# Kernel tuning notes

Measured on AMD Instinct MI355X. Metric: run time of the kernel, lower is better.

The kernel has to match this reference:

```python
import jax, jax.numpy as jnp
import numpy as np

UNITS = 1024
N_CLASSES = 41
SUBSAMPLE = 4
KERNEL = 3
FEAT = 256


def setup_inputs() -> dict:
    key = jax.random.key(0)
    ks = jax.random.split(key, 12)
    B, T, F, U, C = 32, 1000, FEAT, UNITS, N_CLASSES
    s = lambda k, shape, sc: jax.random.normal(k, shape, dtype=jnp.float32) * sc
    return {
        "x": jax.random.normal(ks[0], (B, T, F), dtype=jnp.float32),
        # depthwise conv kernel: (width, 1, channels) for WIO with groups=C
        "conv_w": s(ks[1], (KERNEL, 1, F), 0.1),
        "h0_init": s(ks[2], (1, U), 0.05),
        "w0_x": s(ks[3], (F, 3 * U), 1.0 / np.sqrt(F)),
        "w0_h": s(ks[4], (U, 3 * U), 1.0 / np.sqrt(U)),
        "b0": jnp.zeros((2, 3 * U), dtype=jnp.float32),
        "w1_x": s(ks[5], (U, 3 * U), 1.0 / np.sqrt(U)),
        "w1_h": s(ks[6], (U, 3 * U), 1.0 / np.sqrt(U)),
        "b1": jnp.zeros((2, 3 * U), dtype=jnp.float32),
        "dense_w": s(ks[7], (U, C), 1.0 / np.sqrt(U)),
        "dense_b": jnp.zeros((C,), dtype=jnp.float32),
    }


def _depthwise_conv1d(x, w):
    # x: [B, T, C], w: [K, 1, C]; SAME padding, groups = C, relu, no bias
    C = x.shape[-1]
    y = jax.lax.conv_general_dilated(
        x, w, window_strides=(1,), padding="SAME",
        dimension_numbers=("NWC", "WIO", "NWC"), feature_group_count=C)
    return jax.nn.relu(y)


def _gru_layer(x, h0, Wx, Wh, b):
    # Keras GRU v2 (reset_after=True), gate order z, r, h.
    # x: [B, T, F]; h0: [B, U]; Wx: [F, 3U]; Wh: [U, 3U]; b: [2, 3U]
    xproj = jnp.einsum("btf,fg->btg", x, Wx) + b[0]  # [B, T, 3U]
    br = b[1]

    def step(h, xp):
        rec = h @ Wh + br  # [B, 3U]
        xz, xr, xh = jnp.split(xp, 3, axis=-1)
        rz, rr, rh = jnp.split(rec, 3, axis=-1)
        z = jax.nn.sigmoid(xz + rz)
        r = jax.nn.sigmoid(xr + rr)
        hh = jnp.tanh(xh + r * rh)
        hn = z * h + (1.0 - z) * hh
        return hn, hn

    _, ys = jax.lax.scan(step, h0, jnp.swapaxes(xproj, 0, 1))  # [T, B, U]
    return jnp.swapaxes(ys, 0, 1)


def reference(x, conv_w, h0_init, w0_x, w0_h, b0, w1_x, w1_h, b1, dense_w, dense_b):
    B = x.shape[0]
    U = w0_h.shape[0]
    h = _depthwise_conv1d(x, conv_w)
    # layer 0: learned initial state tiled over batch
    h = _gru_layer(h, jnp.tile(h0_init, (B, 1)), w0_x, w0_h, b0)
    # subsample after layer nLayers-2 == 0
    h = h[:, ::SUBSAMPLE, :]
    # layer 1: zero initial state (Keras default when initial_state is None)
    h = _gru_layer(h, jnp.zeros((B, U), dtype=x.dtype), w1_x, w1_h, b1)
    return h @ dense_w + dense_b  # [B, T//4, nClasses]
```

## Files before the change

kernel.cpp:

```cpp
#include <hip/hip_runtime.h>

typedef unsigned int u32;
typedef unsigned long long u64;
typedef unsigned short u16;
typedef __attribute__((ext_vector_type(8))) short short8;
typedef __attribute__((ext_vector_type(4))) float f32x4;
typedef __attribute__((ext_vector_type(4))) unsigned int u32x4;

#define MFMA(a,b,c) __builtin_amdgcn_mfma_f32_16x16x32_bf16((a),(b),(c),0,0,0)
#define ALOAD32(p)    __hip_atomic_load((p), __ATOMIC_RELAXED, __HIP_MEMORY_SCOPE_AGENT)
#define ASTORE32(p,v) __hip_atomic_store((p),(v), __ATOMIC_RELAXED, __HIP_MEMORY_SCOPE_AGENT)

__device__ __forceinline__ float bf2f(u32 b){ union{u32 u; float f;} v; v.u = b<<16; return v.f; }
__device__ __forceinline__ u16 f2bf(float f){ union{float f; u32 u;} v; v.f = f; u32 u = v.u;
  return (u16)((u + 0x7fffu + ((u>>16)&1u)) >> 16); }
__device__ __forceinline__ u32 pack_f(float v){
  u16 hi = f2bf(v); u16 lo = f2bf(v - bf2f(hi)); return (u32)hi | ((u32)lo<<16); }

__device__ __forceinline__ void unpack8(uint4 a, uint4 b, short8& hi, short8& lo){
  u32 w[8] = {a.x,a.y,a.z,a.w,b.x,b.y,b.z,b.w};
#pragma unroll
  for (int j=0;j<8;++j){ hi[j] = (short)(w[j] & 0xffffu); lo[j] = (short)(w[j] >> 16); }
}
__device__ __forceinline__ void unpackh4(u32x4 a, short8& hi){
#pragma unroll
  for (int i=0;i<4;++i){ hi[2*i] = (short)(a[i] & 0xffffu); hi[2*i+1] = (short)(a[i] >> 16); }
}

constexpr size_t OFF_Y    = 0;
constexpr size_t OFF_SUB  = 32768000;
constexpr size_t OFF_W0IH = 65536000;
constexpr size_t OFF_W0IL = 73400320;
constexpr size_t OFF_W1IH = 81264640;
constexpr size_t OFF_W1IL = 93847552;
constexpr size_t OFF_HB0  = 106430464;
constexpr size_t OFF_HB1  = 106692608;
constexpr size_t OFF_FL0  = 106954752;
constexpr size_t OFF_FL1  = 106955776;
constexpr size_t WS_NEED  = 106956800;

__global__ void build_w0img(const float* __restrict__ w0x, const float* __restrict__ w0h,
                            u16* __restrict__ imgH, u16* __restrict__ imgL){
  for (size_t i = (size_t)blockIdx.x*blockDim.x + threadIdx.x; i < 64ull*61440ull;
       i += (size_t)gridDim.x*blockDim.x){
    int wid = (int)(i / 61440), e = (int)(i % 61440);
    int e2, colbase; const float* src;
    if      (e < 4096) { e2 = e;         colbase = 0;    src = w0x; }
    else if (e < 8192) { e2 = e - 4096;  colbase = 1024; src = w0x; }
    else if (e < 24576){ e2 = e - 8192;  colbase = 0;    src = w0h; }
    else if (e < 40960){ e2 = e - 24576; colbase = 1024; src = w0h; }
    else if (e < 45056){ e2 = e - 40960; colbase = 2048; src = w0x; }
    else               { e2 = e - 45056; colbase = 2048; src = w0h; }
    int blk = e2 >> 9, r = e2 & 511;
    int kseg = r >> 7, c = (r >> 3) & 15, j = r & 7;
    int k = blk*32 + kseg*8 + j;
    int col = colbase + wid*16 + c;
    float v = src[(size_t)k*3072 + col];
    u16 hi = f2bf(v);
    imgH[i] = hi; imgL[i] = f2bf(v - bf2f(hi));
  }
}

__global__ void build_w1img(const float* __restrict__ w1x, const float* __restrict__ w1h,
                            u16* __restrict__ imgH, u16* __restrict__ imgL){
  for (size_t i = (size_t)blockIdx.x*blockDim.x + threadIdx.x; i < 128ull*49152ull;
       i += (size_t)gridDim.x*blockDim.x){
    int wid = (int)(i / 49152), e = (int)(i % 49152);
    int rg = e >> 14, e2 = e & 16383;
    int blk = e2 >> 9, rr = e2 & 511;
    int kseg = rr >> 7, c = (rr >> 3) & 15, j = rr & 7;
    int k = blk*32 + kseg*8 + j;
    const float* src; int col;
    if (rg == 0){ src = w1x; col = (c<8) ? (wid*8+c) : (1024 + wid*8 + c-8); }
    else if (rg == 1){ src = w1h; col = (c<8) ? (wid*8+c) : (1024 + wid*8 + c-8); }
    else { col = 2048 + wid*8 + ((c<8) ? c : c-8); src = (c<8) ? w1x : w1h; }
    float v = src[(size_t)k*3072 + col];
    u16 hi = f2bf(v);
    imgH[i] = hi; imgL[i] = f2bf(v - bf2f(hi));
  }
}

__global__ void init_state(const float* __restrict__ h0, u32* hb0, u32* hb1,
                           int* f0, int* f1){
  int i = blockIdx.x*blockDim.x + threadIdx.x;
  if (i < 256){ f0[i]=0; f1[i]=0; }
  if (i < 16384){
    int p = i & 511;
    u32 v = (u32)f2bf(h0[2*p]) | ((u32)f2bf(h0[2*p+1]) << 16);
    hb0[i] = v;
    hb1[i] = 0u;
  }
}

__global__ void conv_pack(const float* __restrict__ x, const float* __restrict__ cw,
                          u32* __restrict__ yp){
  for (size_t i = (size_t)blockIdx.x*blockDim.x + threadIdx.x; i < 8192000ull;
       i += (size_t)gridDim.x*blockDim.x){
    int f = (int)(i & 255); int b = (int)((i>>8)&31); int t = (int)(i>>13);
    const float* xb = x + ((size_t)b*1000 + t)*256 + f;
    float acc = xb[0]*cw[256+f];
    if (t > 0)   acc += xb[-256]*cw[f];
    if (t < 999) acc += xb[256]*cw[512+f];
    acc = fmaxf(acc, 0.0f);
    yp[i] = pack_f(acc);
  }
}

__global__ __launch_bounds__(512, 1)
void gru16_persist(const u32* __restrict__ xin,
                   const u16* __restrict__ imgH, const u16* __restrict__ imgL,
                   const float* __restrict__ bias,
                   u32* hbuf, int* flags, u32* out_pack)
{
  __shared__ u16 WIMG[61440];
  __shared__ float exch[8*8*66];
  __shared__ float harr[128];
  __shared__ int hready[32];

  const int tid  = threadIdx.x;
  const int wg   = blockIdx.x;
  const int g    = wg >> 6;
  const int wid  = wg & 63;
  const int lane = tid & 63;
  const int wave = tid >> 6;
  const int kq   = wave;
  const int lo16 = lane & 15, hi16 = lane >> 4;
  const int lane_off = hi16*128 + lo16*8;
  const int hsel = (kq >= 4) ? 16 : 0;
  const int srow = lo16 & 7;

  {
    const u64* sH = (const u64*)(imgH + (size_t)wid*61440);
    u64* dH = (u64*)WIMG;
    for (int i = tid; i < 15360; i += 512) dH[i] = sH[i];
    if (tid < 32) hready[tid] = 0;
    if (tid < 128){
      u16 hv = ((const u16*)hbuf)[g*8192 + (tid>>4)*1024 + wid*16 + (tid&15)];
      harr[tid] = bf2f((u32)hv);
    }
  }
  __syncthreads();

  const u16* gLo  = imgL + (size_t)wid*61440;
  const u16* zx_h = &WIMG[kq*512 + lane_off];          const u16* zx_l = gLo + kq*512 + lane_off;
  const u16* rx_h = &WIMG[4096 + kq*512 + lane_off];   const u16* rx_l = gLo + 4096 + kq*512 + lane_off;
  const u16* zh_h = &WIMG[8192 + kq*2048 + lane_off];  const u16* zh_l = gLo + 8192 + kq*2048 + lane_off;
  const u16* rh_h = &WIMG[24576 + kq*2048 + lane_off]; const u16* rh_l = gLo + 24576 + kq*2048 + lane_off;
  const u16* xh_h = &WIMG[40960 + kq*512 + lane_off];  const u16* xh_l = gLo + 40960 + kq*512 + lane_off;
  const u16* hh_h = &WIMG[45056 + kq*2048 + lane_off]; const u16* hh_l = gLo + 45056 + kq*2048 + lane_off;

  const int gs = tid >> 4, gu = tid & 15, eu = wid*16 + gu;
  const float zb  = bias[eu]        + bias[3072 + eu];
  const float rbv = bias[1024 + eu] + bias[4096 + eu];
  const float hxb = bias[2048 + eu];
  const float hrb = bias[5120 + eu];

  for (int t = 0; t < 1000; ++t) {
    const int cur = t & 1, nxt = cur ^ 1;
    f32x4 aZ  = (f32x4){0.f,0.f,0.f,0.f};
    f32x4 aR  = (f32x4){0.f,0.f,0.f,0.f};
    f32x4 aHX = (f32x4){0.f,0.f,0.f,0.f};
    f32x4 aHR = (f32x4){0.f,0.f,0.f,0.f};
    {
      const u32* xr = xin + ((size_t)t*32 + g*8 + srow)*256 + kq*32 + hi16*8;
      uint4 a0 = *(const uint4*)xr;
      uint4 a1 = *(const uint4*)(xr + 4);
      short8 ahi, alo; unpack8(a0, a1, ahi, alo);
      short8 bzh = *(const short8*)zx_h, bzl = *(const short8*)zx_l;
      short8 brh = *(const short8*)rx_h, brl = *(const short8*)rx_l;
      short8 bxh = *(const short8*)xh_h, bxl = *(const short8*)xh_l;
      aZ  = MFMA(ahi,bzh,aZ);  aZ  = MFMA(alo,bzh,aZ);  aZ  = MFMA(ahi,bzl,aZ);
      aR  = MFMA(ahi,brh,aR);  aR  = MFMA(alo,brh,aR);  aR  = MFMA(ahi,brl,aR);
      aHX = MFMA(ahi,bxh,aHX); aHX = MFMA(alo,bxh,aHX); aHX = MFMA(ahi,bxl,aHX);
    }
    if (t > 0) {
      if (wave == 0) {
        int f0;
        do { f0 = ALOAD32(flags + g*64 + (lane & 31)); } while (__all(f0 >= t) == 0);
        asm volatile("" ::: "memory");
        if (lane == 0) ((volatile int*)hready)[0] = t;
      } else if (wave == 1) {
        int f1;
        do { f1 = ALOAD32(flags + g*64 + 32 + (lane & 31)); } while (__all(f1 >= t) == 0);
        asm volatile("" ::: "memory");
        if (lane == 0) ((volatile int*)hready)[16] = t;
      }
      while (((volatile int*)hready)[hsel] < t) { }
      asm volatile("" ::: "memory");
    }
    {
      const u32* hrow = hbuf + cur*16384 + g*4096 + srow*512 + kq*64 + hi16*4;
      u32x4 qa, qb, qc, qd;
      asm volatile(
        "global_load_dwordx4 %0, %4, off sc0 sc1\n\t"
        "global_load_dwordx4 %1, %4, off offset:64 sc0 sc1\n\t"
        "global_load_dwordx4 %2, %4, off offset:128 sc0 sc1\n\t"
        "global_load_dwordx4 %3, %4, off offset:192 sc0 sc1\n\t"
        "s_waitcnt vmcnt(0)"
        : "=&v"(qa), "=&v"(qb), "=&v"(qc), "=&v"(qd)
        : "v"(hrow)
        : "memory");
      short8 ah0, ah1, ah2, ah3;
      unpackh4(qa, ah0); unpackh4(qb, ah1); unpackh4(qc, ah2); unpackh4(qd, ah3);
#pragma unroll
      for (int kt = 0; kt < 4; ++kt){
        short8 ah = (kt==0)?ah0:(kt==1)?ah1:(kt==2)?ah2:ah3;
        short8 bzh = *(const short8*)(zh_h + kt*512), bzl = *(const short8*)(zh_l + kt*512);
        short8 brh = *(const short8*)(rh_h + kt*512), brl = *(const short8*)(rh_l + kt*512);
        short8 bhh = *(const short8*)(hh_h + kt*512), bhl = *(const short8*)(hh_l + kt*512);
        aZ  = MFMA(ah,bzh,aZ);  aZ  = MFMA(ah,bzl,aZ);
        aR  = MFMA(ah,brh,aR);  aR  = MFMA(ah,brl,aR);
        aHR = MFMA(ah,bhh,aHR); aHR = MFMA(ah,bhl,aHR);
      }
    }
    {
      if (hi16 < 2) {
#pragma unroll
        for (int r4 = 0; r4 < 4; ++r4){
          float* e = &exch[(kq*8 + hi16*4 + r4)*66];
          e[lo16]      = aZ[r4];
          e[16 + lo16] = aR[r4];
          e[32 + lo16] = aHX[r4];
          e[48 + lo16] = aHR[r4];
        }
      }
    }
    __syncthreads();
    u32 pk_out = 0;
    if (tid < 128) {
      float zp=0.f, rp=0.f, xh=0.f, rh=0.f;
#pragma unroll
      for (int k8 = 0; k8 < 8; ++k8){
        const float* e = &exch[(k8*8 + gs)*66];
        zp += e[gu]; rp += e[16+gu]; xh += e[32+gu]; rh += e[48+gu];
      }
      float z = 1.f/(1.f + __expf(-(zp + zb)));
      float r = 1.f/(1.f + __expf(-(rp + rbv)));
      float pre = xh + hxb + r*(rh + hrb);
      float ex = __expf(-2.f*fabsf(pre));
      float th = (1.f - ex)/(1.f + ex);
      float hh = copysignf(th, pre);
      float hn = z*harr[tid] + (1.f - z)*hh;
      harr[tid] = hn;
      pk_out = pack_f(hn);
      int pk16 = (int)(pk_out & 0xffffu);
      int prt  = __shfl_xor(pk16, 1);
      if ((tid & 1) == 0) {
        u32 pair = (u32)pk16 | ((u32)prt << 16);
        ASTORE32(hbuf + nxt*16384 + g*4096 + gs*512 + wid*8 + (gu>>1), pair);
      }
    }
    asm volatile("s_waitcnt vmcnt(0)" ::: "memory");
    __syncthreads();
    if (tid == 0)
      ASTORE32(flags + g*64 + wid, t+1);
    if (tid < 128) {
      if ((t & 3) == 0)
        out_pack[((size_t)(t>>2)*32 + g*8 + gs)*1024 + eu] = pk_out;
    }
  }
}

__global__ __launch_bounds__(512, 1)
void gru8L1_persist(const u32* __restrict__ xin,
                    const u16* __restrict__ imgH, const u16* __restrict__ imgL,
                    const float* __restrict__ bias,
                    u32* hbuf, int* flags, u32* out_pack)
{
  __shared__ u16 WIMG[49152];
  __shared__ float exch[8*16*33];
  __shared__ float harr[128];
  __shared__ int hready[32];

  const int tid  = threadIdx.x;
  const int wg   = blockIdx.x;
  const int g    = wg >> 7;
  const int wid  = wg & 127;
  const int lane = tid & 63;
  const int wave = tid >> 6;
  const int kq   = wave;
  const int lo16 = lane & 15, hi16 = lane >> 4;
  const int lane_off = hi16*128 + lo16*8;
  const int hsel = (kq >= 4) ? 16 : 0;

  {
    const u64* sH = (const u64*)(imgH + (size_t)wid*49152);
    u64* dH = (u64*)WIMG;
    for (int i = tid; i < 12288; i += 512) dH[i] = sH[i];
    if (tid < 32) hready[tid] = 0;
    if (tid < 128){
      u16 hv = ((const u16*)hbuf)[g*16384 + (tid>>3)*1024 + wid*8 + (tid&7)];
      harr[tid] = bf2f((u32)hv);
    }
  }
  __syncthreads();

  const u16* gLo   = imgL + (size_t)wid*49152;
  const u16* zrx_h = &WIMG[kq*2048 + lane_off];          const u16* zrx_l = gLo + kq*2048 + lane_off;
  const u16* zrh_h = &WIMG[16384 + kq*2048 + lane_off];  const u16* zrh_l = gLo + 16384 + kq*2048 + lane_off;
  const u16* xhh_h = &WIMG[32768 + kq*2048 + lane_off];  const u16* xhh_l = gLo + 32768 + kq*2048 + lane_off;

  const int gs = tid >> 3, gu = tid & 7, eu = wid*8 + gu;
  const float zb  = bias[eu]        + bias[3072 + eu];
  const float rbv = bias[1024 + eu] + bias[4096 + eu];
  const float hxb = bias[2048 + eu];
  const float hrb = bias[5120 + eu];

  for (int t = 0; t < 250; ++t) {
    const int cur = t & 1, nxt = cur ^ 1;
    f32x4 aZR = (f32x4){0.f,0.f,0.f,0.f};
    f32x4 aXH = (f32x4){0.f,0.f,0.f,0.f};
    f32x4 aHR = (f32x4){0.f,0.f,0.f,0.f};
    {
      const u32* xrow = xin + ((size_t)t*32 + g*16 + lo16)*1024 + kq*128 + hi16*8;
#pragma unroll
      for (int kt = 0; kt < 4; ++kt) {
        uint4 a0 = *(const uint4*)(xrow + kt*32);
        uint4 a1 = *(const uint4*)(xrow + kt*32 + 4);
        short8 ahi, alo; unpack8(a0, a1, ahi, alo);
        short8 bzh = *(const short8*)(zrx_h + kt*512), bzl = *(const short8*)(zrx_l + kt*512);
        short8 bxh = *(const short8*)(xhh_h + kt*512), bxl = *(const short8*)(xhh_l + kt*512);
        aZR = MFMA(ahi,bzh,aZR); aZR = MFMA(alo,bzh,aZR); aZR = MFMA(ahi,bzl,aZR);
        aXH = MFMA(ahi,bxh,aXH); aXH = MFMA(alo,bxh,aXH); aXH = MFMA(ahi,bxl,aXH);
      }
    }
    if (t > 0) {
      if (wave == 0) {
        int f0;
        do { f0 = ALOAD32(flags + g*128 + lane); } while (__all(f0 >= t) == 0);
        asm volatile("" ::: "memory");
        if (lane == 0) ((volatile int*)hready)[0] = t;
      } else if (wave == 1) {
        int f1;
        do { f1 = ALOAD32(flags + g*128 + 64 + lane); } while (__all(f1 >= t) == 0);
        asm volatile("" ::: "memory");
        if (lane == 0) ((volatile int*)hready)[16] = t;
      }
      while (((volatile int*)hready)[hsel] < t) { }
      asm volatile("" ::: "memory");
    }
    {
      const u32* hrow = hbuf + cur*16384 + g*8192 + lo16*512 + kq*64 + hi16*4;
      u32x4 qa, qb, qc, qd;
      asm volatile(
        "global_load_dwordx4 %0, %4, off sc0 sc1\n\t"
        "global_load_dwordx4 %1, %4, off offset:64 sc0 sc1\n\t"
        "global_load_dwordx4 %2, %4, off offset:128 sc0 sc1\n\t"
        "global_load_dwordx4 %3, %4, off offset:192 sc0 sc1\n\t"
        "s_waitcnt vmcnt(0)"
        : "=&v"(qa), "=&v"(qb), "=&v"(qc), "=&v"(qd)
        : "v"(hrow)
        : "memory");
      short8 ah0, ah1, ah2, ah3;
      unpackh4(qa, ah0); unpackh4(qb, ah1); unpackh4(qc, ah2); unpackh4(qd, ah3);
#pragma unroll
      for (int kt = 0; kt < 4; ++kt){
        short8 ah = (kt==0)?ah0:(kt==1)?ah1:(kt==2)?ah2:ah3;
        short8 bzh = *(const short8*)(zrh_h + kt*512), bzl = *(const short8*)(zrh_l + kt*512);
        short8 bhh = *(const short8*)(xhh_h + kt*512), bhl = *(const short8*)(xhh_l + kt*512);
        aZR = MFMA(ah,bzh,aZR); aZR = MFMA(ah,bzl,aZR);
        aHR = MFMA(ah,bhh,aHR); aHR = MFMA(ah,bhl,aHR);
      }
    }
    {
#pragma unroll
      for (int r4 = 0; r4 < 4; ++r4){
        float* e = &exch[(kq*16 + hi16*4 + r4)*33];
        e[lo16]      = aZR[r4];
        e[16 + lo16] = (lo16 < 8) ? aXH[r4] : aHR[r4];
      }
    }
    __syncthreads();
    u32 pk_out = 0;
    if (tid < 128) {
      float zp=0.f, rp=0.f, xh=0.f, rh=0.f;
#pragma unroll
      for (int k8 = 0; k8 < 8; ++k8){
        const float* e = &exch[(k8*16 + gs)*33];
        zp += e[gu]; rp += e[8+gu]; xh += e[16+gu]; rh += e[24+gu];
      }
      float z = 1.f/(1.f + __expf(-(zp + zb)));
      float r = 1.f/(1.f + __expf(-(rp + rbv)));
      float pre = xh + hxb + r*(rh + hrb);
      float ex = __expf(-2.f*fabsf(pre));
      float th = (1.f - ex)/(1.f + ex);
      float hh = copysignf(th, pre);
      float hn = z*harr[tid] + (1.f - z)*hh;
      harr[tid] = hn;
      pk_out = pack_f(hn);
      int pk16 = (int)(pk_out & 0xffffu);
      int prt  = __shfl_xor(pk16, 1);
      if ((tid & 1) == 0) {
        u32 pair = (u32)pk16 | ((u32)prt << 16);
        ASTORE32(hbuf + nxt*16384 + g*8192 + gs*512 + wid*4 + (gu>>1), pair);
      }
    }
    asm volatile("s_waitcnt vmcnt(0)" ::: "memory");
    __syncthreads();
    if (tid == 0)
      ASTORE32(flags + g*128 + wid, t+1);
    if (tid < 128) {
      out_pack[((size_t)t*32 + g*16 + gs)*1024 + eu] = pk_out;
    }
  }
}

__global__ __launch_bounds__(256, 1)
void dense_k(const u32* __restrict__ h2, const float* __restrict__ W,
             const float* __restrict__ bias, float* __restrict__ out){
  __shared__ float rows[32*1025];
  const int ts = blockIdx.x;
  const u32* src = h2 + (size_t)ts*32768;
  for (int i = threadIdx.x; i < 32768; i += 256){
    u32 p = src[i];
    rows[(i>>10)*1025 + (i&1023)] = bf2f(p & 0xffffu) + bf2f(p >> 16);
  }
  __syncthreads();
  const int b = threadIdx.x >> 3, cg = threadIdx.x & 7;
  float acc[6] = {0.f,0.f,0.f,0.f,0.f,0.f};
  for (int k = 0; k < 1024; ++k){
    float hv = rows[b*1025 + k];
    const float* wr = W + k*41;
#pragma unroll
    for (int j = 0; j < 6; ++j){ int c = cg + 8*j; if (c < 41) acc[j] += hv*wr[c]; }
  }
#pragma unroll
  for (int j = 0; j < 6; ++j){
    int c = cg + 8*j;
    if (c < 41) out[((size_t)b*250 + ts)*41 + c] = acc[j] + bias[c];
  }
}

extern "C" void kernel_launch(void* const* d_in, const int* in_sizes, int n_in,
                              void* d_out, int out_size, void* d_ws, size_t ws_size,
                              hipStream_t stream) {
  const float* x      = (const float*)d_in[0];
  const float* conv_w = (const float*)d_in[1];
  const float* h0i    = (const float*)d_in[2];
  const float* w0x    = (const float*)d_in[3];
  const float* w0h    = (const float*)d_in[4];
  const float* b0     = (const float*)d_in[5];
  const float* w1x    = (const float*)d_in[6];
  const float* w1h    = (const float*)d_in[7];
  const float* b1     = (const float*)d_in[8];
  const float* dw     = (const float*)d_in[9];
  const float* db     = (const float*)d_in[10];
  float* outp = (float*)d_out;

  if (ws_size < WS_NEED) return;

  char* ws = (char*)d_ws;
  u32* y_pack   = (u32*)(ws + OFF_Y);
  u32* out2     = (u32*)(ws + OFF_Y);
  u32* sub_pack = (u32*)(ws + OFF_SUB);
  u16* w0iH = (u16*)(ws + OFF_W0IH); u16* w0iL = (u16*)(ws + OFF_W0IL);
  u16* w1iH = (u16*)(ws + OFF_W1IH); u16* w1iL = (u16*)(ws + OFF_W1IL);
  u32* hb0 = (u32*)(ws + OFF_HB0);
  u32* hb1 = (u32*)(ws + OFF_HB1);
  int* fl0 = (int*)(ws + OFF_FL0);
  int* fl1 = (int*)(ws + OFF_FL1);

  init_state<<<64, 512, 0, stream>>>(h0i, hb0, hb1, fl0, fl1);
  build_w0img<<<2048, 256, 0, stream>>>(w0x, w0h, w0iH, w0iL);
  build_w1img<<<2048, 256, 0, stream>>>(w1x, w1h, w1iH, w1iL);
  conv_pack<<<4096, 256, 0, stream>>>(x, conv_w, y_pack);

  gru16_persist<<<256, 512, 0, stream>>>(y_pack, w0iH, w0iL, b0, hb0, fl0, sub_pack);
  gru8L1_persist<<<256, 512, 0, stream>>>(sub_pack, w1iH, w1iL, b1, hb1, fl1, out2);

  dense_k<<<250, 256, 0, stream>>>(out2, dw, db, outp);
}
```

Measured before the change: 5.423 ms.

## Replace second per-step block barrier with LDS flag handshakes in persistent GRU

Removes the trailing __syncthreads after the gate computation in both persistent GRU kernels. In its place it uses LDS flags: the two gate waves signal when they have consumed the exchange buffer, and wave 1 signals when its hidden-state stores have drained. The publish to the global flag is then done by thread 0 after a spin on that signal, and the other waves only wait on the exchange-buffer flag before writing the next step. This shortens the serial per-timestep critical path, at the cost of more subtle spin-based ordering that relies on volatile LDS accesses.

```diff
diff --git a/kernel.cpp b/kernel.cpp
--- a/kernel.cpp
+++ b/kernel.cpp
@@ -106,6 +106,8 @@
   }
 }
 
+#define HREADY_INIT(idx) ((idx)==8 || (idx)==24 || (idx)==25 ? -1 : 0)
+
 __global__ __launch_bounds__(512, 1)
 void gru16_persist(const u32* __restrict__ xin,
                    const u16* __restrict__ imgH, const u16* __restrict__ imgL,
@@ -128,12 +130,13 @@
   const int lane_off = hi16*128 + lo16*8;
   const int hsel = (kq >= 4) ? 16 : 0;
   const int srow = lo16 & 7;
+  volatile int* vh = (volatile int*)hready;
 
   {
     const u64* sH = (const u64*)(imgH + (size_t)wid*61440);
     u64* dH = (u64*)WIMG;
     for (int i = tid; i < 15360; i += 512) dH[i] = sH[i];
-    if (tid < 32) hready[tid] = 0;
+    if (tid < 32) hready[tid] = HREADY_INIT(tid);
     if (tid < 128){
       u16 hv = ((const u16*)hbuf)[g*8192 + (tid>>4)*1024 + wid*16 + (tid&15)];
       harr[tid] = bf2f((u32)hv);
@@ -178,14 +181,14 @@
         int f0;
         do { f0 = ALOAD32(flags + g*64 + (lane & 31)); } while (__all(f0 >= t) == 0);
         asm volatile("" ::: "memory");
-        if (lane == 0) ((volatile int*)hready)[0] = t;
+        if (lane == 0) vh[0] = t;
       } else if (wave == 1) {
         int f1;
         do { f1 = ALOAD32(flags + g*64 + 32 + (lane & 31)); } while (__all(f1 >= t) == 0);
         asm volatile("" ::: "memory");
-        if (lane == 0) ((volatile int*)hready)[16] = t;
-      }
-      while (((volatile int*)hready)[hsel] < t) { }
+        if (lane == 0) vh[16] = t;
+      }
+      while (vh[hsel] < t) { }
       asm volatile("" ::: "memory");
     }
     {
@@ -213,6 +216,8 @@
         aHR = MFMA(ah,bhh,aHR); aHR = MFMA(ah,bhl,aHR);
       }
     }
+    while (vh[8] < t-1 || vh[24] < t-1) { }
+    asm volatile("" ::: "memory");
     {
       if (hi16 < 2) {
 #pragma unroll
@@ -226,7 +231,6 @@
       }
     }
     __syncthreads();
-    u32 pk_out = 0;
     if (tid < 128) {
       float zp=0.f, rp=0.f, xh=0.f, rh=0.f;
 #pragma unroll
@@ -234,6 +238,9 @@
         const float* e = &exch[(k8*8 + gs)*66];
         zp += e[gu]; rp += e[16+gu]; xh += e[32+gu]; rh += e[48+gu];
       }
+      asm volatile("" ::: "memory");
+      if (tid == 0)  vh[8]  = t;
+      if (tid == 64) vh[24] = t;
       float z = 1.f/(1.f + __expf(-(zp + zb)));
       float r = 1.f/(1.f + __expf(-(rp + rbv)));
       float pre = xh + hxb + r*(rh + hrb);
@@ -242,19 +249,19 @@
       float hh = copysignf(th, pre);
       float hn = z*harr[tid] + (1.f - z)*hh;
       harr[tid] = hn;
-      pk_out = pack_f(hn);
+      u32 pk_out = pack_f(hn);
       int pk16 = (int)(pk_out & 0xffffu);
       int prt  = __shfl_xor(pk16, 1);
       if ((tid & 1) == 0) {
         u32 pair = (u32)pk16 | ((u32)prt << 16);
         ASTORE32(hbuf + nxt*16384 + g*4096 + gs*512 + wid*8 + (gu>>1), pair);
       }
-    }
-    asm volatile("s_waitcnt vmcnt(0)" ::: "memory");
-    __syncthreads();
-    if (tid == 0)
-      ASTORE32(flags + g*64 + wid, t+1);
-    if (tid < 128) {
+      asm volatile("s_waitcnt vmcnt(0)" ::: "memory");
+      if (tid == 64) vh[25] = t;
+      if (tid == 0) {
+        while (vh[25] < t) { }
+        ASTORE32(flags + g*64 + wid, t+1);
+      }
       if ((t & 3) == 0)
         out_pack[((size_t)(t>>2)*32 + g*8 + gs)*1024 + eu] = pk_out;
     }
@@ -282,12 +289,13 @@
   const int lo16 = lane & 15, hi16 = lane >> 4;
   const int lane_off = hi16*128 + lo16*8;
   const int hsel = (kq >= 4) ? 16 : 0;
+  volatile int* vh = (volatile int*)hready;
 
   {
     const u64* sH = (const u64*)(imgH + (size_t)wid*49152);
     u64* dH = (u64*)WIMG;
     for (int i = tid; i < 12288; i += 512) dH[i] = sH[i];
-    if (tid < 32) hready[tid] = 0;
+    if (tid < 32) hready[tid] = HREADY_INIT(tid);
     if (tid < 128){
       u16 hv = ((const u16*)hbuf)[g*16384 + (tid>>3)*1024 + wid*8 + (tid&7)];
       harr[tid] = bf2f((u32)hv);
@@ -329,14 +337,14 @@
         int f0;
         do { f0 = ALOAD32(flags + g*128 + lane); } while (__all(f0 >= t) == 0);
         asm volatile("" ::: "memory");
-        if (lane == 0) ((volatile int*)hready)[0] = t;
+        if (lane == 0) vh[0] = t;
       } else if (wave == 1) {
         int f1;
         do { f1 = ALOAD32(flags + g*128 + 64 + lane); } while (__all(f1 >= t) == 0);
         asm volatile("" ::: "memory");
-        if (lane == 0) ((volatile int*)hready)[16] = t;
-      }
-      while (((volatile int*)hready)[hsel] < t) { }
+        if (lane == 0) vh[16] = t;
+      }
+      while (vh[hsel] < t) { }
       asm volatile("" ::: "memory");
     }
     {
@@ -362,6 +370,8 @@
         aHR = MFMA(ah,bhh,aHR); aHR = MFMA(ah,bhl,aHR);
       }
     }
+    while (vh[8] < t-1 || vh[24] < t-1) { }
+    asm volatile("" ::: "memory");
     {
 #pragma unroll
       for (int r4 = 0; r4 < 4; ++r4){
@@ -371,7 +381,6 @@
       }
     }
     __syncthreads();
-    u32 pk_out = 0;
     if (tid < 128) {
       float zp=0.f, rp=0.f, xh=0.f, rh=0.f;
 #pragma unroll
@@ -379,6 +388,9 @@
         const float* e = &exch[(k8*16 + gs)*33];
         zp += e[gu]; rp += e[8+gu]; xh += e[16+gu]; rh += e[24+gu];
       }
+      asm volatile("" ::: "memory");
+      if (tid == 0)  vh[8]  = t;
+      if (tid == 64) vh[24] = t;
       float z = 1.f/(1.f + __expf(-(zp + zb)));
       float r = 1.f/(1.f + __expf(-(rp + rbv)));
       float pre = xh + hxb + r*(rh + hrb);
@@ -387,19 +399,19 @@
       float hh = copysignf(th, pre);
       float hn = z*harr[tid] + (1.f - z)*hh;
       harr[tid] = hn;
-      pk_out = pack_f(hn);
+      u32 pk_out = pack_f(hn);
       int pk16 = (int)(pk_out & 0xffffu);
       int prt  = __shfl_xor(pk16, 1);
       if ((tid & 1) == 0) {
         u32 pair = (u32)pk16 | ((u32)prt << 16);
         ASTORE32(hbuf + nxt*16384 + g*8192 + gs*512 + wid*4 + (gu>>1), pair);
       }
-    }
-    asm volatile("s_waitcnt vmcnt(0)" ::: "memory");
-    __syncthreads();
-    if (tid == 0)
-      ASTORE32(flags + g*128 + wid, t+1);
-    if (tid < 128) {
+      asm volatile("s_waitcnt vmcnt(0)" ::: "memory");
+      if (tid == 64) vh[25] = t;
+      if (tid == 0) {
+        while (vh[25] < t) { }
+        ASTORE32(flags + g*128 + wid, t+1);
+      }
       out_pack[((size_t)t*32 + g*16 + gs)*1024 + eu] = pk_out;
     }
   }
```

Result: slower. 6.008 ms (+10.8%).
